# Kernel tuning notes

Hardware: AMD Instinct MI355X
Metric: run time of the kernel (lower is better)

Reference implementation:

```python
import jax, jax.numpy as jnp
import numpy as np

DMODEL = 512
NUM_HEADS = 8
DK = DMODEL // NUM_HEADS  # 64
CAUSAL = True


def setup_inputs() -> dict:
    key = jax.random.key(0)
    ks = jax.random.split(key, 11)
    B, S = 4, 2048
    s_in = 1.0 / np.sqrt(DMODEL)
    s_out = 1.0 / np.sqrt(NUM_HEADS * DK)
    return {
        "Q": jax.random.normal(ks[0], (B, S, DMODEL), jnp.float32),
        "K": jax.random.normal(ks[1], (B, S, DMODEL), jnp.float32),
        "V": jax.random.normal(ks[2], (B, S, DMODEL), jnp.float32),
        # torch nn.Linear weights stored as [in, out] (already transposed)
        "WQ_w": jax.random.uniform(ks[3], (DMODEL, DK), jnp.float32, -s_in, s_in),
        "WQ_b": jax.random.uniform(ks[4], (DK,), jnp.float32, -s_in, s_in),
        "WK_w": jax.random.uniform(ks[5], (DMODEL, DK), jnp.float32, -s_in, s_in),
        "WK_b": jax.random.uniform(ks[6], (DK,), jnp.float32, -s_in, s_in),
        "WV_w": jax.random.uniform(ks[7], (DMODEL, DK), jnp.float32, -s_in, s_in),
        "WV_b": jax.random.uniform(ks[8], (DK,), jnp.float32, -s_in, s_in),
        "Wo_w": jax.random.uniform(ks[9], (NUM_HEADS * DK, DMODEL), jnp.float32, -s_out, s_out),
        "Wo_b": jax.random.uniform(ks[10], (DMODEL,), jnp.float32, -s_out, s_out),
    }


def reference(Q, K, V, WQ_w, WQ_b, WK_w, WK_b, WV_w, WV_b, Wo_w, Wo_b):
    # Single shared projection to dk=64 (NOT per-head in the original module)
    q = Q @ WQ_w + WQ_b  # [B,S,dk]
    k = K @ WK_w + WK_b  # [B,S,dk]
    v = V @ WV_w + WV_b  # [B,S,dk]
    scores = jnp.einsum("bsd,btd->bst", q, k) / np.sqrt(DK).astype(np.float32)
    if CAUSAL:
        S = scores.shape[-1]
        causal = jnp.tril(jnp.ones((S, S), dtype=bool))  # True = keep
        scores = jnp.where(causal, scores, -jnp.inf)
    attn = jax.nn.softmax(scores, axis=-1)
    head_out = jnp.einsum("bst,btd->bsd", attn, v)  # [B,S,dk]
    # Every head is identical -> concat == tile num_heads copies
    concat = jnp.tile(head_out, (1, 1, NUM_HEADS))  # [B,S,num_heads*dk]
    return concat @ Wo_w + Wo_b  # [B,S,dmodel]
```

## Files before the change

### kernel.cpp

```cpp
#include <hip/hip_runtime.h>
#include <hip/hip_bf16.h>

#define DMODEL 512
#define DK 64
#define NH 8
#define SEQ 2048
#define BATCH 4
#define NROWS 8192
#define NEGBIG -1.0e30f
#define SPLITW 8
#define DKP 66
#define SHIFT 6.0f

typedef _Float16 half_t;
typedef _Float16 half8 __attribute__((ext_vector_type(8)));
typedef _Float16 half4 __attribute__((ext_vector_type(4)));
typedef float floatx4 __attribute__((ext_vector_type(4)));

#if defined(__has_builtin)
#if __has_builtin(__builtin_amdgcn_mfma_f32_16x16x16f16)
#define HAVE_MFMA16X16X16 1
#else
#define HAVE_MFMA16X16X16 0
#endif
#else
#define HAVE_MFMA16X16X16 0
#endif

__global__ __launch_bounds__(256) void prep_kernel(
    const float* __restrict__ WQ, const float* __restrict__ WK,
    const float* __restrict__ WV, const float* __restrict__ Wo,
    half_t* __restrict__ wtq, half_t* __restrict__ wtk, half_t* __restrict__ wtv,
    half_t* __restrict__ wo_tr)
{
    const int idx = blockIdx.x * 256 + threadIdx.x;
    const int n = idx >> 9;
    const int k = idx & 511;
    wtq[idx] = (half_t)WQ[k * DK + n];
    wtk[idx] = (half_t)WK[k * DK + n];
    wtv[idx] = (half_t)WV[k * DK + n];
    const int n2 = idx >> 6;
    const int k2 = idx & 63;
    float s = 0.f;
#pragma unroll
    for (int h = 0; h < NH; h++)
        s += Wo[((size_t)(h * DK + k2)) * DMODEL + n2];
    wo_tr[idx] = (half_t)s;
}

__global__ __launch_bounds__(128) void proj_kernel(
    const float* __restrict__ Q, const float* __restrict__ K, const float* __restrict__ V,
    const half_t* __restrict__ wtq, const half_t* __restrict__ wtk, const half_t* __restrict__ wtv,
    const float* __restrict__ bQ, const float* __restrict__ bK, const float* __restrict__ bV,
    half_t* __restrict__ qh, half_t* __restrict__ kh, half_t* __restrict__ vt)
{
    const int tens = blockIdx.y;
    const float* X  = (tens == 0) ? Q : (tens == 1) ? K : V;
    const half_t* wt = (tens == 0) ? wtq : (tens == 1) ? wtk : wtv;
    const float* bias = (tens == 0) ? bQ : (tens == 1) ? bK : bV;

    const int r0 = blockIdx.x * 16;
    const int tid = threadIdx.x;
    const int w = tid >> 6;
    const int lane = tid & 63;
    const int c = lane & 15;
    const int quad = lane >> 4;

    __shared__ floatx4 red[4][64];

    floatx4 acc[4] = {{0.f,0.f,0.f,0.f},{0.f,0.f,0.f,0.f},{0.f,0.f,0.f,0.f},{0.f,0.f,0.f,0.f}};

    const float* xrow = X + (size_t)(r0 + c) * DMODEL + quad * 8;
#pragma unroll 8
    for (int ks = w; ks < 16; ks += 2) {
        const float* xp = xrow + ks * 32;
        half8 a;
#pragma unroll
        for (int i = 0; i < 8; i++) a[i] = (half_t)xp[i];
#pragma unroll
        for (int nt = 0; nt < 4; nt++) {
            half8 bfr = *(const half8*)(wt + (size_t)(nt * 16 + c) * DMODEL + ks * 32 + quad * 8);
            acc[nt] = __builtin_amdgcn_mfma_f32_16x16x32_f16(a, bfr, acc[nt], 0, 0, 0);
        }
    }

    if (w == 1) {
#pragma unroll
        for (int nt = 0; nt < 4; nt++) red[nt][lane] = acc[nt];
    }
    __syncthreads();
    if (w == 1) return;

#pragma unroll
    for (int nt = 0; nt < 4; nt++) {
        const floatx4 r4 = red[nt][lane];
        const float bv = bias[nt * 16 + c];
#pragma unroll
        for (int r = 0; r < 4; r++) {
            const float val = acc[nt][r] + r4[r] + bv;
            const int row = r0 + quad * 4 + r;
            if (tens == 0) {
                qh[(size_t)row * DK + nt * 16 + c] = (half_t)val;
            } else if (tens == 1) {
                kh[(size_t)row * DK + nt * 16 + c] = (half_t)val;
            } else {
                const int b  = row >> 11;
                const int s  = row & (SEQ - 1);
                const int kb = s >> 4;
                const int kk = s & 15;
                vt[((((size_t)b * 128 + kb) * 4 + nt) * 16 + c) * 16 + kk] = (half_t)val;
            }
        }
    }
}

__global__ __launch_bounds__(512, 4) void attn_kernel(
    const half_t* __restrict__ qh, const half_t* __restrict__ kh,
    const half_t* __restrict__ vt, const half_t* __restrict__ wo_tr,
    const float* __restrict__ bo, float* __restrict__ out)
{
    const int bx = blockIdx.x;
    int b, qt;
    if (bx < 256) { qt = bx >> 1;            b = bx & 1; }
    else          { int k2 = bx - 256; qt = 127 - (k2 >> 1); b = 2 + (k2 & 1); }
    const int tid = threadIdx.x;
    const int w = tid >> 6;
    const int lane = tid & 63;
    const int c = lane & 15;
    const int quad = lane >> 4;

    __shared__ float sow[SPLITW][16][DKP];
    __shared__ float sl_s[SPLITW][16];
    __shared__ half_t of16[16][72];

    const half_t* qrow = qh + (size_t)(b * SEQ + qt * 16 + c) * DK + quad * 8;
    half8 qb0 = *(const half8*)(qrow);
    half8 qb1 = *(const half8*)(qrow + 32);
#pragma unroll
    for (int i = 0; i < 8; i++) { qb0[i] = qb0[i] * (half_t)0.125f; qb1[i] = qb1[i] * (half_t)0.125f; }

    float lp = 0.f;
    floatx4 o[4] = {{0.f,0.f,0.f,0.f},{0.f,0.f,0.f,0.f},{0.f,0.f,0.f,0.f},{0.f,0.f,0.f,0.f}};
    const floatx4 cinit = {-SHIFT, -SHIFT, -SHIFT, -SHIFT};

    const half_t* kbb = kh + (size_t)b * SEQ * DK;
    const half_t* vtb = vt + (size_t)b * 128 * 1024;

    int pb = w;
    half8 ka0, ka1, kb0, kb1;
    if (2 * pb <= qt) {
        const half_t* kr0 = kbb + (size_t)(2 * pb * 16 + c) * DK + quad * 8;
        ka0 = *(const half8*)(kr0);
        ka1 = *(const half8*)(kr0 + 32);
        const half_t* kr1 = kr0 + 16 * DK;
        kb0 = *(const half8*)(kr1);
        kb1 = *(const half8*)(kr1 + 32);
    }

    while (2 * pb <= qt) {
        const int t0 = 2 * pb, t1 = 2 * pb + 1;
        const half_t* vk0 = vtb + (size_t)t0 * 1024;
        const half_t* vk1 = vtb + (size_t)t1 * 1024;
#if HAVE_MFMA16X16X16
        half4 va0 = *(const half4*)(vk0 + ((size_t)0 * 16 + c) * 16 + quad * 4);
        half4 va1 = *(const half4*)(vk0 + ((size_t)1 * 16 + c) * 16 + quad * 4);
        half4 va2 = *(const half4*)(vk0 + ((size_t)2 * 16 + c) * 16 + quad * 4);
        half4 va3 = *(const half4*)(vk0 + ((size_t)3 * 16 + c) * 16 + quad * 4);
        half4 vc0 = *(const half4*)(vk1 + ((size_t)0 * 16 + c) * 16 + quad * 4);
        half4 vc1 = *(const half4*)(vk1 + ((size_t)1 * 16 + c) * 16 + quad * 4);
        half4 vc2 = *(const half4*)(vk1 + ((size_t)2 * 16 + c) * 16 + quad * 4);
        half4 vc3 = *(const half4*)(vk1 + ((size_t)3 * 16 + c) * 16 + quad * 4);
#else
        half8 va80 = *(const half8*)(vk0 + ((size_t)0 * 16 + c) * 16 + (quad & 1) * 8);
        half8 va81 = *(const half8*)(vk0 + ((size_t)1 * 16 + c) * 16 + (quad & 1) * 8);
        half8 va82 = *(const half8*)(vk0 + ((size_t)2 * 16 + c) * 16 + (quad & 1) * 8);
        half8 va83 = *(const half8*)(vk0 + ((size_t)3 * 16 + c) * 16 + (quad & 1) * 8);
        half8 vc80 = *(const half8*)(vk1 + ((size_t)0 * 16 + c) * 16 + (quad & 1) * 8);
        half8 vc81 = *(const half8*)(vk1 + ((size_t)1 * 16 + c) * 16 + (quad & 1) * 8);
        half8 vc82 = *(const half8*)(vk1 + ((size_t)2 * 16 + c) * 16 + (quad & 1) * 8);
        half8 vc83 = *(const half8*)(vk1 + ((size_t)3 * 16 + c) * 16 + (quad & 1) * 8);
#endif
        const int npb = pb + SPLITW;
        half8 nka0 = ka0, nka1 = ka1, nkb0 = kb0, nkb1 = kb1;
        if (2 * npb <= qt) {
            const half_t* nkr0 = kbb + (size_t)(2 * npb * 16 + c) * DK + quad * 8;
            nka0 = *(const half8*)(nkr0);
            nka1 = *(const half8*)(nkr0 + 32);
            const half_t* nkr1 = nkr0 + 16 * DK;
            nkb0 = *(const half8*)(nkr1);
            nkb1 = *(const half8*)(nkr1 + 32);
        }

        floatx4 sc0 = cinit;
        sc0 = __builtin_amdgcn_mfma_f32_16x16x32_f16(ka0, qb0, sc0, 0, 0, 0);
        sc0 = __builtin_amdgcn_mfma_f32_16x16x32_f16(ka1, qb1, sc0, 0, 0, 0);
        floatx4 sc1 = cinit;
        sc1 = __builtin_amdgcn_mfma_f32_16x16x32_f16(kb0, qb0, sc1, 0, 0, 0);
        sc1 = __builtin_amdgcn_mfma_f32_16x16x32_f16(kb1, qb1, sc1, 0, 0, 0);

        if (t0 == qt) {
#pragma unroll
            for (int r = 0; r < 4; r++) {
                if (quad * 4 + r > c) sc0[r] = NEGBIG;
                sc1[r] = NEGBIG;
            }
        } else if (t1 == qt) {
#pragma unroll
            for (int r = 0; r < 4; r++)
                if (quad * 4 + r > c) sc1[r] = NEGBIG;
        }

        float p0[4], p1[4];
#pragma unroll
        for (int r = 0; r < 4; r++) { p0[r] = __expf(sc0[r]); p1[r] = __expf(sc1[r]); }
        lp += (p0[0] + p0[1] + p0[2] + p0[3]) + (p1[0] + p1[1] + p1[2] + p1[3]);

#if HAVE_MFMA16X16X16
        half4 pa, pc;
#pragma unroll
        for (int r = 0; r < 4; r++) { pa[r] = (half_t)p0[r]; pc[r] = (half_t)p1[r]; }
        o[0] = __builtin_amdgcn_mfma_f32_16x16x16f16(pa, va0, o[0], 0, 0, 0);
        o[1] = __builtin_amdgcn_mfma_f32_16x16x16f16(pa, va1, o[1], 0, 0, 0);
        o[2] = __builtin_amdgcn_mfma_f32_16x16x16f16(pa, va2, o[2], 0, 0, 0);
        o[3] = __builtin_amdgcn_mfma_f32_16x16x16f16(pa, va3, o[3], 0, 0, 0);
        o[0] = __builtin_amdgcn_mfma_f32_16x16x16f16(pc, vc0, o[0], 0, 0, 0);
        o[1] = __builtin_amdgcn_mfma_f32_16x16x16f16(pc, vc1, o[1], 0, 0, 0);
        o[2] = __builtin_amdgcn_mfma_f32_16x16x16f16(pc, vc2, o[2], 0, 0, 0);
        o[3] = __builtin_amdgcn_mfma_f32_16x16x16f16(pc, vc3, o[3], 0, 0, 0);
#else
        half8 pa8, pc8;
#pragma unroll
        for (int j = 0; j < 8; j++) {
            const int src = (((quad * 2 + (j >> 2)) & 3) * 16 + c);
            const float pj0 = __shfl(p0[j & 3], src);
            const float pj1 = __shfl(p1[j & 3], src);
            pa8[j] = (quad < 2) ? (half_t)pj0 : (half_t)0.f;
            pc8[j] = (quad < 2) ? (half_t)pj1 : (half_t)0.f;
        }
        o[0] = __builtin_amdgcn_mfma_f32_16x16x32_f16(pa8, va80, o[0], 0, 0, 0);
        o[1] = __builtin_amdgcn_mfma_f32_16x16x32_f16(pa8, va81, o[1], 0, 0, 0);
        o[2] = __builtin_amdgcn_mfma_f32_16x16x32_f16(pa8, va82, o[2], 0, 0, 0);
        o[3] = __builtin_amdgcn_mfma_f32_16x16x32_f16(pa8, va83, o[3], 0, 0, 0);
        o[0] = __builtin_amdgcn_mfma_f32_16x16x32_f16(pc8, vc80, o[0], 0, 0, 0);
        o[1] = __builtin_amdgcn_mfma_f32_16x16x32_f16(pc8, vc81, o[1], 0, 0, 0);
        o[2] = __builtin_amdgcn_mfma_f32_16x16x32_f16(pc8, vc82, o[2], 0, 0, 0);
        o[3] = __builtin_amdgcn_mfma_f32_16x16x32_f16(pc8, vc83, o[3], 0, 0, 0);
#endif
        ka0 = nka0; ka1 = nka1; kb0 = nkb0; kb1 = nkb1; pb = npb;
    }

    lp += __shfl_xor(lp, 16);
    lp += __shfl_xor(lp, 32);

#pragma unroll
    for (int nt = 0; nt < 4; nt++)
#pragma unroll
        for (int r = 0; r < 4; r++)
            sow[w][quad * 4 + r][nt * 16 + c] = o[nt][r];
    if (quad == 0) sl_s[w][c] = lp;
    __syncthreads();

    {
        const int q = w * 2 + (lane >> 5);
        const int d0 = (lane & 31) * 2;
        float lstar = 0.f, acc0 = 0.f, acc1 = 0.f;
#pragma unroll
        for (int ww = 0; ww < SPLITW; ww++) {
            lstar += sl_s[ww][q];
            const float* sp = &sow[ww][q][d0];
            acc0 += sp[0];
            acc1 += sp[1];
        }
        const float linv = 1.f / lstar;
        of16[q][d0]     = (half_t)(acc0 * linv);
        of16[q][d0 + 1] = (half_t)(acc1 * linv);
    }
    __syncthreads();

    half8 a1 = *(const half8*)(&of16[c][quad * 8]);
    half8 a2 = *(const half8*)(&of16[c][32 + quad * 8]);
    const size_t orow = (size_t)(b * SEQ + qt * 16);
#pragma unroll
    for (int i = 0; i < 4; i++) {
        const int n = (w * 4 + i) * 16 + c;
        half8 b1 = *(const half8*)(wo_tr + (size_t)n * DK + quad * 8);
        half8 b2 = *(const half8*)(wo_tr + (size_t)n * DK + 32 + quad * 8);
        floatx4 oc = {0.f, 0.f, 0.f, 0.f};
        oc = __builtin_amdgcn_mfma_f32_16x16x32_f16(a1, b1, oc, 0, 0, 0);
        oc = __builtin_amdgcn_mfma_f32_16x16x32_f16(a2, b2, oc, 0, 0, 0);
        const float bv = bo[n];
#pragma unroll
        for (int r = 0; r < 4; r++)
            out[(orow + quad * 4 + r) * DMODEL + n] = oc[r] + bv;
    }
}

extern "C" void kernel_launch(void* const* d_in, const int* in_sizes, int n_in,
                              void* d_out, int out_size, void* d_ws, size_t ws_size,
                              hipStream_t stream) {
    const float* Q  = (const float*)d_in[0];
    const float* K  = (const float*)d_in[1];
    const float* V  = (const float*)d_in[2];
    const float* WQ = (const float*)d_in[3];
    const float* bQ = (const float*)d_in[4];
    const float* WK = (const float*)d_in[5];
    const float* bK = (const float*)d_in[6];
    const float* WV = (const float*)d_in[7];
    const float* bV = (const float*)d_in[8];
    const float* Wo = (const float*)d_in[9];
    const float* bo = (const float*)d_in[10];
    float* out = (float*)d_out;

    char* ws = (char*)d_ws;
    half_t* qh    = (half_t*)ws;
    half_t* kh    = (half_t*)(ws + (1u << 20));
    half_t* vt    = (half_t*)(ws + (2u << 20));
    half_t* wtq   = (half_t*)(ws + (3u << 20));
    half_t* wtk   = wtq + 32768;
    half_t* wtv   = wtk + 32768;
    half_t* wo_tr = wtv + 32768;

    prep_kernel<<<128, 256, 0, stream>>>(WQ, WK, WV, Wo, wtq, wtk, wtv, wo_tr);
    proj_kernel<<<dim3(512, 3), 128, 0, stream>>>(Q, K, V, wtq, wtk, wtv, bQ, bK, bV, qh, kh, vt);
    attn_kernel<<<512, 512, 0, stream>>>(qh, kh, vt, wo_tr, bo, out);
}
```

Measured before the change: 141.0 us.

## Fold softmax scale into Q projection, use exp2, and widen V loads

Folds the 1/sqrt(dk)·log2(e) scale into the Q projection output so the attention kernel drops its per-element Q scaling and can use a native exp2 instead of expf. The shift constant is rescaled to match. The V tile layout is reorganised so each lane fetches its four 16x16 V fragments with two 16-byte loads instead of eight 8-byte loads. Probabilities are also packed to fp16 with the pkrtz conversion. The prep kernel's transposes are reindexed to make the reads coalesced. The risks are slightly different rounding, since Q is scaled before the fp16 cast, and round-toward-zero packing.

```diff
diff --git a/kernel.cpp b/kernel.cpp
--- a/kernel.cpp
+++ b/kernel.cpp
@@ -1,5 +1,4 @@
 #include <hip/hip_runtime.h>
-#include <hip/hip_bf16.h>
 
 #define DMODEL 512
 #define DK 64
@@ -10,22 +9,47 @@
 #define NEGBIG -1.0e30f
 #define SPLITW 8
 #define DKP 66
-#define SHIFT 6.0f
+#define SHIFT2 8.656170245f
+#define QSCALE 0.1803368801f
 
 typedef _Float16 half_t;
+typedef _Float16 half4 __attribute__((ext_vector_type(4)));
 typedef _Float16 half8 __attribute__((ext_vector_type(8)));
-typedef _Float16 half4 __attribute__((ext_vector_type(4)));
 typedef float floatx4 __attribute__((ext_vector_type(4)));
 
-#if defined(__has_builtin)
-#if __has_builtin(__builtin_amdgcn_mfma_f32_16x16x16f16)
-#define HAVE_MFMA16X16X16 1
+#ifdef __has_builtin
+#  if __has_builtin(__builtin_amdgcn_exp2f)
+#    define EXP2F(x) __builtin_amdgcn_exp2f(x)
+#  endif
+#  if __has_builtin(__builtin_amdgcn_cvt_pkrtz)
+#    define HAVE_PKRTZ 1
+#  endif
+#  if __has_builtin(__builtin_amdgcn_mfma_f32_16x16x16f16)
+#    define HAVE_MFMA16 1
+#  endif
+#endif
+#ifndef EXP2F
+#  define EXP2F(x) exp2f(x)
+#endif
+#ifndef HAVE_PKRTZ
+#  define HAVE_PKRTZ 0
+#endif
+#ifndef HAVE_MFMA16
+#  define HAVE_MFMA16 0
+#endif
+
+__device__ __forceinline__ half4 pk4(const float* p) {
+#if HAVE_PKRTZ
+    half4 r;
+    auto lo = __builtin_amdgcn_cvt_pkrtz(p[0], p[1]);
+    auto hi = __builtin_amdgcn_cvt_pkrtz(p[2], p[3]);
+    __builtin_memcpy(&r, &lo, 4);
+    __builtin_memcpy(reinterpret_cast<char*>(&r) + 4, &hi, 4);
+    return r;
 #else
-#define HAVE_MFMA16X16X16 0
-#endif
-#else
-#define HAVE_MFMA16X16X16 0
-#endif
+    return (half4){(half_t)p[0], (half_t)p[1], (half_t)p[2], (half_t)p[3]};
+#endif
+}
 
 __global__ __launch_bounds__(256) void prep_kernel(
     const float* __restrict__ WQ, const float* __restrict__ WK,
@@ -34,18 +58,18 @@
     half_t* __restrict__ wo_tr)
 {
     const int idx = blockIdx.x * 256 + threadIdx.x;
-    const int n = idx >> 9;
-    const int k = idx & 511;
-    wtq[idx] = (half_t)WQ[k * DK + n];
-    wtk[idx] = (half_t)WK[k * DK + n];
-    wtv[idx] = (half_t)WV[k * DK + n];
-    const int n2 = idx >> 6;
-    const int k2 = idx & 63;
+    const int k = idx >> 6;
+    const int n = idx & 63;
+    wtq[(size_t)n * DMODEL + k] = (half_t)WQ[idx];
+    wtk[(size_t)n * DMODEL + k] = (half_t)WK[idx];
+    wtv[(size_t)n * DMODEL + k] = (half_t)WV[idx];
+    const int n2 = idx & 511;
+    const int k2 = idx >> 9;
     float s = 0.f;
 #pragma unroll
     for (int h = 0; h < NH; h++)
         s += Wo[((size_t)(h * DK + k2)) * DMODEL + n2];
-    wo_tr[idx] = (half_t)s;
+    wo_tr[(size_t)n2 * DK + k2] = (half_t)s;
 }
 
 __global__ __launch_bounds__(128) void proj_kernel(
@@ -100,7 +124,7 @@
             const float val = acc[nt][r] + r4[r] + bv;
             const int row = r0 + quad * 4 + r;
             if (tens == 0) {
-                qh[(size_t)row * DK + nt * 16 + c] = (half_t)val;
+                qh[(size_t)row * DK + nt * 16 + c] = (half_t)(val * QSCALE);
             } else if (tens == 1) {
                 kh[(size_t)row * DK + nt * 16 + c] = (half_t)val;
             } else {
@@ -108,7 +132,9 @@
                 const int s  = row & (SEQ - 1);
                 const int kb = s >> 4;
                 const int kk = s & 15;
-                vt[((((size_t)b * 128 + kb) * 4 + nt) * 16 + c) * 16 + kk] = (half_t)val;
+                vt[(size_t)(b * 128 + kb) * 1024
+                   + (size_t)c * 64 + (nt >> 1) * 32 + (kk >> 2) * 8 + (nt & 1) * 4 + (kk & 3)]
+                    = (half_t)val;
             }
         }
     }
@@ -136,12 +162,10 @@
     const half_t* qrow = qh + (size_t)(b * SEQ + qt * 16 + c) * DK + quad * 8;
     half8 qb0 = *(const half8*)(qrow);
     half8 qb1 = *(const half8*)(qrow + 32);
-#pragma unroll
-    for (int i = 0; i < 8; i++) { qb0[i] = qb0[i] * (half_t)0.125f; qb1[i] = qb1[i] * (half_t)0.125f; }
 
     float lp = 0.f;
     floatx4 o[4] = {{0.f,0.f,0.f,0.f},{0.f,0.f,0.f,0.f},{0.f,0.f,0.f,0.f},{0.f,0.f,0.f,0.f}};
-    const floatx4 cinit = {-SHIFT, -SHIFT, -SHIFT, -SHIFT};
+    const floatx4 cinit = {-SHIFT2, -SHIFT2, -SHIFT2, -SHIFT2};
 
     const half_t* kbb = kh + (size_t)b * SEQ * DK;
     const half_t* vtb = vt + (size_t)b * 128 * 1024;
@@ -159,27 +183,13 @@
 
     while (2 * pb <= qt) {
         const int t0 = 2 * pb, t1 = 2 * pb + 1;
-        const half_t* vk0 = vtb + (size_t)t0 * 1024;
-        const half_t* vk1 = vtb + (size_t)t1 * 1024;
-#if HAVE_MFMA16X16X16
-        half4 va0 = *(const half4*)(vk0 + ((size_t)0 * 16 + c) * 16 + quad * 4);
-        half4 va1 = *(const half4*)(vk0 + ((size_t)1 * 16 + c) * 16 + quad * 4);
-        half4 va2 = *(const half4*)(vk0 + ((size_t)2 * 16 + c) * 16 + quad * 4);
-        half4 va3 = *(const half4*)(vk0 + ((size_t)3 * 16 + c) * 16 + quad * 4);
-        half4 vc0 = *(const half4*)(vk1 + ((size_t)0 * 16 + c) * 16 + quad * 4);
-        half4 vc1 = *(const half4*)(vk1 + ((size_t)1 * 16 + c) * 16 + quad * 4);
-        half4 vc2 = *(const half4*)(vk1 + ((size_t)2 * 16 + c) * 16 + quad * 4);
-        half4 vc3 = *(const half4*)(vk1 + ((size_t)3 * 16 + c) * 16 + quad * 4);
-#else
-        half8 va80 = *(const half8*)(vk0 + ((size_t)0 * 16 + c) * 16 + (quad & 1) * 8);
-        half8 va81 = *(const half8*)(vk0 + ((size_t)1 * 16 + c) * 16 + (quad & 1) * 8);
-        half8 va82 = *(const half8*)(vk0 + ((size_t)2 * 16 + c) * 16 + (quad & 1) * 8);
-        half8 va83 = *(const half8*)(vk0 + ((size_t)3 * 16 + c) * 16 + (quad & 1) * 8);
-        half8 vc80 = *(const half8*)(vk1 + ((size_t)0 * 16 + c) * 16 + (quad & 1) * 8);
-        half8 vc81 = *(const half8*)(vk1 + ((size_t)1 * 16 + c) * 16 + (quad & 1) * 8);
-        half8 vc82 = *(const half8*)(vk1 + ((size_t)2 * 16 + c) * 16 + (quad & 1) * 8);
-        half8 vc83 = *(const half8*)(vk1 + ((size_t)3 * 16 + c) * 16 + (quad & 1) * 8);
-#endif
+        const half_t* vp0 = vtb + (size_t)t0 * 1024 + c * 64 + quad * 8;
+        const half_t* vp1 = vtb + (size_t)t1 * 1024 + c * 64 + quad * 8;
+        half8 va01 = *(const half8*)(vp0);
+        half8 va23 = *(const half8*)(vp0 + 32);
+        half8 vc01 = *(const half8*)(vp1);
+        half8 vc23 = *(const half8*)(vp1 + 32);
+
         const int npb = pb + SPLITW;
         half8 nka0 = ka0, nka1 = ka1, nkb0 = kb0, nkb1 = kb1;
         if (2 * npb <= qt) {
@@ -212,13 +222,19 @@
 
         float p0[4], p1[4];
 #pragma unroll
-        for (int r = 0; r < 4; r++) { p0[r] = __expf(sc0[r]); p1[r] = __expf(sc1[r]); }
-        lp += (p0[0] + p0[1] + p0[2] + p0[3]) + (p1[0] + p1[1] + p1[2] + p1[3]);
-
-#if HAVE_MFMA16X16X16
-        half4 pa, pc;
-#pragma unroll
-        for (int r = 0; r < 4; r++) { pa[r] = (half_t)p0[r]; pc[r] = (half_t)p1[r]; }
+        for (int r = 0; r < 4; r++) { p0[r] = EXP2F(sc0[r]); p1[r] = EXP2F(sc1[r]); }
+        lp += (p0[0] + p0[1]) + (p0[2] + p0[3]) + ((p1[0] + p1[1]) + (p1[2] + p1[3]));
+
+#if HAVE_MFMA16
+        half4 pa = pk4(p0), pc = pk4(p1);
+        half4 va0 = __builtin_shufflevector(va01, va01, 0, 1, 2, 3);
+        half4 va1 = __builtin_shufflevector(va01, va01, 4, 5, 6, 7);
+        half4 va2 = __builtin_shufflevector(va23, va23, 0, 1, 2, 3);
+        half4 va3 = __builtin_shufflevector(va23, va23, 4, 5, 6, 7);
+        half4 vc0 = __builtin_shufflevector(vc01, vc01, 0, 1, 2, 3);
+        half4 vc1 = __builtin_shufflevector(vc01, vc01, 4, 5, 6, 7);
+        half4 vc2 = __builtin_shufflevector(vc23, vc23, 0, 1, 2, 3);
+        half4 vc3 = __builtin_shufflevector(vc23, vc23, 4, 5, 6, 7);
         o[0] = __builtin_amdgcn_mfma_f32_16x16x16f16(pa, va0, o[0], 0, 0, 0);
         o[1] = __builtin_amdgcn_mfma_f32_16x16x16f16(pa, va1, o[1], 0, 0, 0);
         o[2] = __builtin_amdgcn_mfma_f32_16x16x16f16(pa, va2, o[2], 0, 0, 0);
@@ -230,21 +246,26 @@
 #else
         half8 pa8, pc8;
 #pragma unroll
-        for (int j = 0; j < 8; j++) {
-            const int src = (((quad * 2 + (j >> 2)) & 3) * 16 + c);
-            const float pj0 = __shfl(p0[j & 3], src);
-            const float pj1 = __shfl(p1[j & 3], src);
-            pa8[j] = (quad < 2) ? (half_t)pj0 : (half_t)0.f;
-            pc8[j] = (quad < 2) ? (half_t)pj1 : (half_t)0.f;
-        }
-        o[0] = __builtin_amdgcn_mfma_f32_16x16x32_f16(pa8, va80, o[0], 0, 0, 0);
-        o[1] = __builtin_amdgcn_mfma_f32_16x16x32_f16(pa8, va81, o[1], 0, 0, 0);
-        o[2] = __builtin_amdgcn_mfma_f32_16x16x32_f16(pa8, va82, o[2], 0, 0, 0);
-        o[3] = __builtin_amdgcn_mfma_f32_16x16x32_f16(pa8, va83, o[3], 0, 0, 0);
-        o[0] = __builtin_amdgcn_mfma_f32_16x16x32_f16(pc8, vc80, o[0], 0, 0, 0);
-        o[1] = __builtin_amdgcn_mfma_f32_16x16x32_f16(pc8, vc81, o[1], 0, 0, 0);
-        o[2] = __builtin_amdgcn_mfma_f32_16x16x32_f16(pc8, vc82, o[2], 0, 0, 0);
-        o[3] = __builtin_amdgcn_mfma_f32_16x16x32_f16(pc8, vc83, o[3], 0, 0, 0);
+        for (int jj = 0; jj < 8; jj++) {
+            const int src = (((quad * 2 + (jj >> 2)) & 3) * 16 + c);
+            const float pj0 = __shfl(p0[jj & 3], src);
+            const float pj1 = __shfl(p1[jj & 3], src);
+            pa8[jj] = (quad < 2) ? (half_t)pj0 : (half_t)0.f;
+            pc8[jj] = (quad < 2) ? (half_t)pj1 : (half_t)0.f;
+        }
+#pragma unroll
+        for (int nt = 0; nt < 4; nt++) {
+            const half_t* vb0 = vtb + (size_t)t0 * 1024 + c * 64 + (nt >> 1) * 32 + (quad & 1) * 16 + (nt & 1) * 4;
+            half4 l0 = *(const half4*)(vb0);
+            half4 h0 = *(const half4*)(vb0 + 8);
+            half8 v80 = {l0[0], l0[1], l0[2], l0[3], h0[0], h0[1], h0[2], h0[3]};
+            o[nt] = __builtin_amdgcn_mfma_f32_16x16x32_f16(pa8, v80, o[nt], 0, 0, 0);
+            const half_t* vb1 = vtb + (size_t)t1 * 1024 + c * 64 + (nt >> 1) * 32 + (quad & 1) * 16 + (nt & 1) * 4;
+            half4 l1 = *(const half4*)(vb1);
+            half4 h1 = *(const half4*)(vb1 + 8);
+            half8 v81 = {l1[0], l1[1], l1[2], l1[3], h1[0], h1[1], h1[2], h1[3]};
+            o[nt] = __builtin_amdgcn_mfma_f32_16x16x32_f16(pc8, v81, o[nt], 0, 0, 0);
+        }
 #endif
         ka0 = nka0; ka1 = nka1; kb0 = nkb0; kb1 = nkb1; pb = npb;
     }
```

New measurement: 142.0 us. No clear change (+0.7%).
